# Optimization experiments

Hardware: AMD Instinct MI355X
Metric: run time of the kernel (lower is better)

The kernel has to match this reference:

```python
import jax, jax.numpy as jnp
import numpy as np

T, N, D, E, O = 2, 4096, 1024, 8, 1024

def setup_inputs() -> dict:
    key = jax.random.key(0)
    k1, k2, k3 = jax.random.split(key, 3)
    x = jax.random.normal(k1, (T, N, D), dtype=jnp.float32)
    Wg = jax.random.normal(k2, (T, D, E), dtype=jnp.float32) * (1.0 / np.sqrt(D))
    We = jax.random.normal(k3, (E, D, O), dtype=jnp.float32) * (1.0 / np.sqrt(D))
    return {"x": x, "Wg": Wg, "We": We, "k": 2}


def reference(x, Wg, We, k):
    # Per-task gating logits: [T, N, E]
    logits = jnp.einsum('tnd,tde->tne', x, Wg)
    # Top-k mask per token (scatter 1.0 at top-k indices)
    _, topk_idx = jax.lax.top_k(logits, k)                      # [T, N, k]
    mask = jax.nn.one_hot(topk_idx, E, dtype=logits.dtype).sum(-2)  # [T, N, E]
    masked = mask * logits
    gates = masked / (masked.sum(-1, keepdims=True) + 1e-9)     # [T, N, E]
    # Dense expert outputs (each expert is Linear(D, O)): [T, N, E, O]
    eout = jnp.einsum('tnd,edo->tneo', x, We)
    # Weighted combine over selected experts
    out = jnp.einsum('tne,tneo->tno', gates, eout)              # [T, N, O]
    return out
```

## Files before the change

### kernel.cpp

```cpp
#include <hip/hip_runtime.h>
#include <hip/hip_bf16.h>
#include <stdint.h>

#define T_ 2
#define N_ 4096
#define D_ 1024
#define E_ 8
#define O_ 1024

#define BM 128
#define BN 128
#define BK 32

typedef __attribute__((ext_vector_type(8))) short short8;
typedef __attribute__((ext_vector_type(4))) float f32x4;

#define AS1 __attribute__((address_space(1)))
#define AS3 __attribute__((address_space(3)))

__device__ inline void gld16(const unsigned short* g, unsigned short* l) {
    __builtin_amdgcn_global_load_lds((const AS1 unsigned int*)g,
                                     (AS3 unsigned int*)l, 16, 0, 0);
}

__device__ inline unsigned short f2bf(float f) {
    union { float f; unsigned u; } v; v.f = f;
    unsigned r = v.u + 0x7fff + ((v.u >> 16) & 1);
    return (unsigned short)(r >> 16);
}

__global__ __launch_bounds__(256) void gate_kernel(
    const float* __restrict__ x, const float* __restrict__ Wg,
    unsigned short* __restrict__ xb,
    int* __restrict__ route, float2* __restrict__ gpair)
{
    __shared__ __align__(16) float WgT[E_][D_];

    int tid = threadIdx.x;
    int wave = tid >> 6, lane = tid & 63;
    int token0 = blockIdx.x * 8;
    int t = token0 >> 12;
    const float* wgb = Wg + (size_t)t * D_ * E_;

#pragma unroll
    for (int r = 0; r < 8; ++r) {
        int f = r * 1024 + tid * 4;
        float4 v = *(const float4*)(wgb + f);
        WgT[f & 7][f >> 3]             = v.x;
        WgT[(f + 1) & 7][(f + 1) >> 3] = v.y;
        WgT[(f + 2) & 7][(f + 2) >> 3] = v.z;
        WgT[(f + 3) & 7][(f + 3) >> 3] = v.w;
    }
    __syncthreads();

#pragma unroll
    for (int tl = 0; tl < 2; ++tl) {
        int token = token0 + wave * 2 + tl;
        const float* xrow = x + (size_t)token * D_;

        float4 xv[4];
#pragma unroll
        for (int c = 0; c < 4; ++c)
            xv[c] = *(const float4*)(xrow + c * 256 + lane * 4);

        float acc[E_] = {0.f, 0.f, 0.f, 0.f, 0.f, 0.f, 0.f, 0.f};
#pragma unroll
        for (int c = 0; c < 4; ++c) {
            int d0 = c * 256 + lane * 4;
            unsigned lo = f2bf(xv[c].x) | ((unsigned)f2bf(xv[c].y) << 16);
            unsigned hi = f2bf(xv[c].z) | ((unsigned)f2bf(xv[c].w) << 16);
            *(uint2*)(&xb[(size_t)token * D_ + d0]) = make_uint2(lo, hi);
#pragma unroll
            for (int e = 0; e < E_; ++e) {
                float4 w = *(const float4*)(&WgT[e][d0]);
                acc[e] += xv[c].x * w.x + xv[c].y * w.y + xv[c].z * w.z + xv[c].w * w.w;
            }
        }
#pragma unroll
        for (int off = 1; off < 64; off <<= 1) {
#pragma unroll
            for (int e = 0; e < E_; ++e) acc[e] += __shfl_xor(acc[e], off, 64);
        }

        if (lane == 0) {
            float best = acc[0]; int bi = 0;
#pragma unroll
            for (int e = 1; e < E_; ++e) if (acc[e] > best) { best = acc[e]; bi = e; }
            float sec = -INFINITY; int si = 0;
#pragma unroll
            for (int e = 0; e < E_; ++e) if (e != bi && acc[e] > sec) { sec = acc[e]; si = e; }
            float s = best + sec + 1e-9f;
            route[token] = bi | (si << 8);
            gpair[token] = make_float2(best / s, sec / s);
        }
    }
}

__global__ __launch_bounds__(256) void build_lists(
    const int* __restrict__ route, const float2* __restrict__ gpair,
    int* __restrict__ toklist, float* __restrict__ gatelist,
    int* __restrict__ counts)
{
    int g = blockIdx.x;
    int t = g >> 3, e = g & 7;
    int tid = threadIdx.x;
    int wave = tid >> 6, lane = tid & 63;

    __shared__ int waveSum[4];
    __shared__ int base;
    if (tid == 0) base = 0;

    for (int c = 0; c < N_; c += 256) {
        int n = c + tid;
        int r = route[t * N_ + n];
        int e0 = r & 255, e1 = (r >> 8) & 255;
        bool sel = (e0 == e) || (e1 == e);
        unsigned long long b = __ballot(sel);
        int pre  = __popcll(b & ((1ull << lane) - 1ull));
        if (lane == 0) waveSum[wave] = __popcll(b);
        __syncthreads();
        int woff = 0;
#pragma unroll
        for (int w = 0; w < 4; ++w) woff += (w < wave) ? waveSum[w] : 0;
        int total = waveSum[0] + waveSum[1] + waveSum[2] + waveSum[3];
        if (sel) {
            int p = base + woff + pre;
            int slot = (e0 == e) ? 0 : 1;
            toklist[g * N_ + p] = n | (slot << 16);
            float2 gp = gpair[t * N_ + n];
            gatelist[g * N_ + p] = (e0 == e) ? gp.x : gp.y;
        }
        __syncthreads();
        if (tid == 0) base += total;
    }
    __syncthreads();
    if (tid == 0) counts[g] = base;
}

__global__ __launch_bounds__(256) void pack_kernel(
    const float* __restrict__ We, unsigned short* __restrict__ Wbp)
{
    __shared__ __align__(16) unsigned short P[64 * 136];

    int b = blockIdx.x;
    int e  = b >> 7;
    int oy = (b & 127) >> 3;
    int dz = b & 7;
    int o0 = oy * 64, d0 = dz * 128;
    int tid = threadIdx.x;

#pragma unroll
    for (int r = 0; r < 32; ++r) {
        int lin = r * 256 + tid;
        int dd = lin >> 6, oo = lin & 63;
        P[oo * 136 + dd] = f2bf(We[((size_t)(e * D_ + d0 + dd)) * O_ + o0 + oo]);
    }
    __syncthreads();

#pragma unroll
    for (int w = 0; w < 4; ++w) {
        int ci = w * 256 + tid;
        int oo = ci >> 4, dc = ci & 15;
        uint4 v = *(const uint4*)&P[oo * 136 + dc * 8];
        int o = o0 + oo;
        int ot = o >> 7, nn = o & 127;
        unsigned short* dst =
            Wbp + ((size_t)((e * 8 + ot) * 128 + nn)) * D_ + d0 + dc * 8;
        *(uint4*)dst = v;
    }
}

__global__ __launch_bounds__(256) void moe_gemm(
    const unsigned short* __restrict__ xb,
    const unsigned short* __restrict__ Wbp,
    const int* __restrict__ toklist, const float* __restrict__ gatelist,
    const int* __restrict__ counts, float* __restrict__ out)
{
    int lin = blockIdx.x;
    int mt  = lin >> 7;
    int u   = lin & 127;
    int xcd = u & 7;
    int v   = u >> 3;
    int g   = 2 * xcd + (v >> 3);
    int ot  = v & 7;
    int t   = g >> 3;

    int cnt = counts[g];
    int m0 = mt * BM;
    if (m0 >= cnt) return;

    __shared__ __align__(16) unsigned short As[BM * BK];
    __shared__ __align__(16) unsigned short Bs[BN * BK];
    __shared__ int   tokS[BM];
    __shared__ float gateS[BM];

    int tid = threadIdx.x;
    if (tid < BM) {
        int r = m0 + tid;
        tokS[tid]  = (r < cnt) ? toklist[g * N_ + r]  : -1;
        gateS[tid] = (r < cnt) ? gatelist[g * N_ + r] : 0.f;
    }
    __syncthreads();

    int wave = tid >> 6, lane = tid & 63;
    int lr = lane >> 2;
    int sg = (lane & 3) ^ (lr & 3);
    int c0 = wave * 2, c1 = c0 + 1;
    int ar0 = c0 * 16 + lr, ar1 = c1 * 16 + lr;
    int tok0 = max(tokS[ar0], 0) & 0xFFFF;
    int tok1 = max(tokS[ar1], 0) & 0xFFFF;
    const unsigned short* ag0 = xb + ((size_t)(t * N_ + tok0)) * D_ + sg * 8;
    const unsigned short* ag1 = xb + ((size_t)(t * N_ + tok1)) * D_ + sg * 8;
    const unsigned short* wb  = Wbp + ((size_t)((g & 7) * 8 + ot) * 128) * D_;
    const unsigned short* bg0 = wb + (size_t)ar0 * D_ + sg * 8;
    const unsigned short* bg1 = wb + (size_t)ar1 * D_ + sg * 8;
    unsigned short* la0 = &As[c0 * 512];
    unsigned short* la1 = &As[c1 * 512];
    unsigned short* lb0 = &Bs[c0 * 512];
    unsigned short* lb1 = &Bs[c1 * 512];

    int fr = lane & 15, q = lane >> 4;
    int wm = (wave & 1) * 64, wn = (wave >> 1) * 64;
    int fp = (q ^ (fr & 3)) * 8;

    f32x4 acc[4][4];
#pragma unroll
    for (int mi = 0; mi < 4; ++mi)
#pragma unroll
        for (int ni = 0; ni < 4; ++ni) acc[mi][ni] = (f32x4){0.f, 0.f, 0.f, 0.f};

    for (int k0 = 0; k0 < D_; k0 += BK) {
        gld16(ag0 + k0, la0);
        gld16(ag1 + k0, la1);
        gld16(bg0 + k0, lb0);
        gld16(bg1 + k0, lb1);
        __syncthreads();

        short8 af[4], bf[4];
#pragma unroll
        for (int mi = 0; mi < 4; ++mi)
            af[mi] = *(const short8*)(&As[(wm + mi * 16 + fr) * BK + fp]);
#pragma unroll
        for (int ni = 0; ni < 4; ++ni)
            bf[ni] = *(const short8*)(&Bs[(wn + ni * 16 + fr) * BK + fp]);
#pragma unroll
        for (int mi = 0; mi < 4; ++mi)
#pragma unroll
            for (int ni = 0; ni < 4; ++ni)
                acc[mi][ni] = __builtin_amdgcn_mfma_f32_16x16x32_bf16(
                    af[mi], bf[ni], acc[mi][ni], 0, 0, 0);
        __syncthreads();
    }

    float* outb = out + (size_t)t * N_ * O_;
    int ncol = ot * 128 + wn + fr;
#pragma unroll
    for (int mi = 0; mi < 4; ++mi) {
#pragma unroll
        for (int r = 0; r < 4; ++r) {
            int ml = wm + mi * 16 + q * 4 + r;
            int ent = tokS[ml];
            if (ent >= 0) {
                int tok  = ent & 0xFFFF;
                int slot = ent >> 16;
                float gate = gateS[ml];
#pragma unroll
                for (int ni = 0; ni < 4; ++ni) {
                    unsigned short* p =
                        (unsigned short*)(outb + (size_t)tok * O_ + ncol + ni * 16);
                    p[slot] = f2bf(gate * acc[mi][ni][r]);
                }
            }
        }
    }
}

__global__ __launch_bounds__(256) void combine_kernel(float* __restrict__ out)
{
    size_t i = ((size_t)blockIdx.x * 256 + threadIdx.x) * 4;
    unsigned* po = (unsigned*)out;
    uint4 v = *(uint4*)(po + i);
    float4 r;
    union { unsigned u; float f; } a, b;
#define CMB(comp, src) a.u = (src) << 16; b.u = (src) & 0xFFFF0000u; comp = a.f + b.f
    CMB(r.x, v.x); CMB(r.y, v.y); CMB(r.z, v.z); CMB(r.w, v.w);
#undef CMB
    *(float4*)(out + i) = r;
}

extern "C" void kernel_launch(void* const* d_in, const int* in_sizes, int n_in,
                              void* d_out, int out_size, void* d_ws, size_t ws_size,
                              hipStream_t stream)
{
    const float* x  = (const float*)d_in[0];
    const float* Wg = (const float*)d_in[1];
    const float* We = (const float*)d_in[2];
    float* out = (float*)d_out;

    char* ws = (char*)d_ws;
    unsigned short* xb   = (unsigned short*)(ws);
    unsigned short* Wbp  = (unsigned short*)(ws + 16777216);
    int*   toklist       = (int*)  (ws + 33554432);
    float* gatelist      = (float*)(ws + 33816576);
    int*   counts        = (int*)  (ws + 34078720);
    int*   route         = (int*)  (ws + 34078976);
    float2* gpair        = (float2*)(ws + 34111744);

    gate_kernel<<<(T_ * N_) / 8, 256, 0, stream>>>(x, Wg, xb, route, gpair);
    build_lists<<<T_ * E_, 256, 0, stream>>>(route, gpair, toklist, gatelist, counts);
    pack_kernel<<<E_ * (O_ / 64) * (D_ / 128), 256, 0, stream>>>(We, Wbp);
    moe_gemm<<<(N_ / BM) * 8 * (T_ * E_), 256, 0, stream>>>(
        xb, Wbp, toklist, gatelist, counts, out);
    combine_kernel<<<((size_t)T_ * N_ * O_) / (256 * 4), 256, 0, stream>>>(out);
}
```

Measured before the change: 194.7 us.

## Double-buffer LDS tiles in expert GEMM and adjust LDS swizzle

The A and B LDS tiles become ping-pong buffers. The next k-slice's global-to-LDS loads are issued after the current fragments are read into registers, so loads overlap with the MFMA work, and one barrier per iteration is removed. The XOR swizzle for LDS writes and fragment reads changes from row&3 to (row>>1)&3 to reduce bank conflicts on short8 reads. This doubles tile LDS use, which may lower occupancy, and it relies on the barrier waiting for the async LDS loads to finish.

```diff
diff --git a/kernel.cpp b/kernel.cpp
--- a/kernel.cpp
+++ b/kernel.cpp
@@ -189,8 +189,8 @@
     int m0 = mt * BM;
     if (m0 >= cnt) return;
 
-    __shared__ __align__(16) unsigned short As[BM * BK];
-    __shared__ __align__(16) unsigned short Bs[BN * BK];
+    __shared__ __align__(16) unsigned short As[2][BM * BK];
+    __shared__ __align__(16) unsigned short Bs[2][BN * BK];
     __shared__ int   tokS[BM];
     __shared__ float gateS[BM];
 
@@ -204,7 +204,7 @@
 
     int wave = tid >> 6, lane = tid & 63;
     int lr = lane >> 2;
-    int sg = (lane & 3) ^ (lr & 3);
+    int sg = (lane & 3) ^ ((lane >> 3) & 3);
     int c0 = wave * 2, c1 = c0 + 1;
     int ar0 = c0 * 16 + lr, ar1 = c1 * 16 + lr;
     int tok0 = max(tokS[ar0], 0) & 0xFFFF;
@@ -214,14 +214,10 @@
     const unsigned short* wb  = Wbp + ((size_t)((g & 7) * 8 + ot) * 128) * D_;
     const unsigned short* bg0 = wb + (size_t)ar0 * D_ + sg * 8;
     const unsigned short* bg1 = wb + (size_t)ar1 * D_ + sg * 8;
-    unsigned short* la0 = &As[c0 * 512];
-    unsigned short* la1 = &As[c1 * 512];
-    unsigned short* lb0 = &Bs[c0 * 512];
-    unsigned short* lb1 = &Bs[c1 * 512];
 
     int fr = lane & 15, q = lane >> 4;
     int wm = (wave & 1) * 64, wn = (wave >> 1) * 64;
-    int fp = (q ^ (fr & 3)) * 8;
+    int fp = (q ^ ((fr >> 1) & 3)) * 8;
 
     f32x4 acc[4][4];
 #pragma unroll
@@ -229,27 +225,37 @@
 #pragma unroll
         for (int ni = 0; ni < 4; ++ni) acc[mi][ni] = (f32x4){0.f, 0.f, 0.f, 0.f};
 
-    for (int k0 = 0; k0 < D_; k0 += BK) {
-        gld16(ag0 + k0, la0);
-        gld16(ag1 + k0, la1);
-        gld16(bg0 + k0, lb0);
-        gld16(bg1 + k0, lb1);
+    gld16(ag0, &As[0][c0 * 512]);
+    gld16(ag1, &As[0][c1 * 512]);
+    gld16(bg0, &Bs[0][c0 * 512]);
+    gld16(bg1, &Bs[0][c1 * 512]);
+
+    for (int k = 0; k < D_ / BK; ++k) {
+        int p = k & 1;
         __syncthreads();
 
         short8 af[4], bf[4];
 #pragma unroll
         for (int mi = 0; mi < 4; ++mi)
-            af[mi] = *(const short8*)(&As[(wm + mi * 16 + fr) * BK + fp]);
+            af[mi] = *(const short8*)(&As[p][(wm + mi * 16 + fr) * BK + fp]);
 #pragma unroll
         for (int ni = 0; ni < 4; ++ni)
-            bf[ni] = *(const short8*)(&Bs[(wn + ni * 16 + fr) * BK + fp]);
+            bf[ni] = *(const short8*)(&Bs[p][(wn + ni * 16 + fr) * BK + fp]);
+
+        if (k + 1 < D_ / BK) {
+            int ko = (k + 1) * BK;
+            gld16(ag0 + ko, &As[p ^ 1][c0 * 512]);
+            gld16(ag1 + ko, &As[p ^ 1][c1 * 512]);
+            gld16(bg0 + ko, &Bs[p ^ 1][c0 * 512]);
+            gld16(bg1 + ko, &Bs[p ^ 1][c1 * 512]);
+        }
+
 #pragma unroll
         for (int mi = 0; mi < 4; ++mi)
 #pragma unroll
             for (int ni = 0; ni < 4; ++ni)
                 acc[mi][ni] = __builtin_amdgcn_mfma_f32_16x16x32_bf16(
                     af[mi], bf[ni], acc[mi][ni], 0, 0, 0);
-        __syncthreads();
     }
 
     float* outb = out + (size_t)t * N_ * O_;
@@ -266,9 +272,9 @@
                 float gate = gateS[ml];
 #pragma unroll
                 for (int ni = 0; ni < 4; ++ni) {
-                    unsigned short* p =
+                    unsigned short* p2 =
                         (unsigned short*)(outb + (size_t)tok * O_ + ncol + ni * 16);
-                    p[slot] = f2bf(gate * acc[mi][ni][r]);
+                    p2[slot] = f2bf(gate * acc[mi][ni][r]);
                 }
             }
         }
```

Result: no change. 198.1 us (+1.7%).

## Widen GEMM N tile to 256 and switch to 32x32x16 MFMA

Applied to the files above, without the earlier changes.

The grouped MoE GEMM tile grows from 128x128 to 128x256, so each block loads an A tile once for twice as many output columns. The MFMA shape changes from 16x16x32 to 32x32x16, and the LDS swizzle and epilogue row mapping are reworked to match. The packed weight layout becomes plain row-major per expert, and the launch bounds now request two blocks per CU. The larger tile raises register and LDS use per block and halves the number of blocks, which may reduce occupancy and parallelism when per-expert token counts are small.

```diff
diff --git a/kernel.cpp b/kernel.cpp
--- a/kernel.cpp
+++ b/kernel.cpp
@@ -9,11 +9,11 @@
 #define O_ 1024
 
 #define BM 128
-#define BN 128
+#define BN2 256
 #define BK 32
 
 typedef __attribute__((ext_vector_type(8))) short short8;
-typedef __attribute__((ext_vector_type(4))) float f32x4;
+typedef __attribute__((ext_vector_type(16))) float f32x16;
 
 #define AS1 __attribute__((address_space(1)))
 #define AS3 __attribute__((address_space(3)))
@@ -163,26 +163,24 @@
         int oo = ci >> 4, dc = ci & 15;
         uint4 v = *(const uint4*)&P[oo * 136 + dc * 8];
         int o = o0 + oo;
-        int ot = o >> 7, nn = o & 127;
-        unsigned short* dst =
-            Wbp + ((size_t)((e * 8 + ot) * 128 + nn)) * D_ + d0 + dc * 8;
+        unsigned short* dst = Wbp + ((size_t)(e * O_ + o)) * D_ + d0 + dc * 8;
         *(uint4*)dst = v;
     }
 }
 
-__global__ __launch_bounds__(256) void moe_gemm(
+__global__ __launch_bounds__(256, 2) void moe_gemm(
     const unsigned short* __restrict__ xb,
     const unsigned short* __restrict__ Wbp,
     const int* __restrict__ toklist, const float* __restrict__ gatelist,
     const int* __restrict__ counts, float* __restrict__ out)
 {
     int lin = blockIdx.x;
-    int mt  = lin >> 7;
-    int u   = lin & 127;
+    int mt  = lin >> 6;
+    int u   = lin & 63;
     int xcd = u & 7;
     int v   = u >> 3;
-    int g   = 2 * xcd + (v >> 3);
-    int ot  = v & 7;
+    int g   = 2 * xcd + (v >> 2);
+    int ot  = v & 3;
     int t   = g >> 3;
 
     int cnt = counts[g];
@@ -190,7 +188,7 @@
     if (m0 >= cnt) return;
 
     __shared__ __align__(16) unsigned short As[BM * BK];
-    __shared__ __align__(16) unsigned short Bs[BN * BK];
+    __shared__ __align__(16) unsigned short Bs[BN2 * BK];
     __shared__ int   tokS[BM];
     __shared__ float gateS[BM];
 
@@ -204,71 +202,78 @@
 
     int wave = tid >> 6, lane = tid & 63;
     int lr = lane >> 2;
-    int sg = (lane & 3) ^ (lr & 3);
-    int c0 = wave * 2, c1 = c0 + 1;
-    int ar0 = c0 * 16 + lr, ar1 = c1 * 16 + lr;
-    int tok0 = max(tokS[ar0], 0) & 0xFFFF;
-    int tok1 = max(tokS[ar1], 0) & 0xFFFF;
-    const unsigned short* ag0 = xb + ((size_t)(t * N_ + tok0)) * D_ + sg * 8;
-    const unsigned short* ag1 = xb + ((size_t)(t * N_ + tok1)) * D_ + sg * 8;
-    const unsigned short* wb  = Wbp + ((size_t)((g & 7) * 8 + ot) * 128) * D_;
-    const unsigned short* bg0 = wb + (size_t)ar0 * D_ + sg * 8;
-    const unsigned short* bg1 = wb + (size_t)ar1 * D_ + sg * 8;
-    unsigned short* la0 = &As[c0 * 512];
-    unsigned short* la1 = &As[c1 * 512];
-    unsigned short* lb0 = &Bs[c0 * 512];
-    unsigned short* lb1 = &Bs[c1 * 512];
-
-    int fr = lane & 15, q = lane >> 4;
-    int wm = (wave & 1) * 64, wn = (wave >> 1) * 64;
-    int fp = (q ^ (fr & 3)) * 8;
-
-    f32x4 acc[4][4];
-#pragma unroll
-    for (int mi = 0; mi < 4; ++mi)
-#pragma unroll
-        for (int ni = 0; ni < 4; ++ni) acc[mi][ni] = (f32x4){0.f, 0.f, 0.f, 0.f};
+    int sg = (lane & 3) ^ ((lane >> 3) & 3);
+    int a0 = wave * 32 + lr, a1 = a0 + 16;
+    int tokA0 = max(tokS[a0], 0) & 0xFFFF;
+    int tokA1 = max(tokS[a1], 0) & 0xFFFF;
+    const unsigned short* ag0 = xb + ((size_t)(t * N_ + tokA0)) * D_ + sg * 8;
+    const unsigned short* ag1 = xb + ((size_t)(t * N_ + tokA1)) * D_ + sg * 8;
+    const unsigned short* wb  = Wbp + ((size_t)((g & 7) * O_ + ot * BN2)) * D_;
+    const unsigned short* bg[4];
+#pragma unroll
+    for (int i = 0; i < 4; ++i)
+        bg[i] = wb + (size_t)(wave * 64 + i * 16 + lr) * D_ + sg * 8;
+
+    int fm = lane & 31, kg = lane >> 5;
+    int wm = (wave & 1) * 64, wn = (wave >> 1) * 128;
+    int sA = (fm >> 1) & 3;
+
+    f32x16 acc[2][4];
+#pragma unroll
+    for (int mi = 0; mi < 2; ++mi)
+#pragma unroll
+        for (int ni = 0; ni < 4; ++ni)
+#pragma unroll
+            for (int r = 0; r < 16; ++r) acc[mi][ni][r] = 0.f;
 
     for (int k0 = 0; k0 < D_; k0 += BK) {
-        gld16(ag0 + k0, la0);
-        gld16(ag1 + k0, la1);
-        gld16(bg0 + k0, lb0);
-        gld16(bg1 + k0, lb1);
+        gld16(ag0 + k0, &As[(wave * 2) * 512]);
+        gld16(ag1 + k0, &As[(wave * 2 + 1) * 512]);
+#pragma unroll
+        for (int i = 0; i < 4; ++i)
+            gld16(bg[i] + k0, &Bs[(wave * 4 + i) * 512]);
         __syncthreads();
 
-        short8 af[4], bf[4];
-#pragma unroll
-        for (int mi = 0; mi < 4; ++mi)
-            af[mi] = *(const short8*)(&As[(wm + mi * 16 + fr) * BK + fp]);
-#pragma unroll
-        for (int ni = 0; ni < 4; ++ni)
-            bf[ni] = *(const short8*)(&Bs[(wn + ni * 16 + fr) * BK + fp]);
-#pragma unroll
-        for (int mi = 0; mi < 4; ++mi)
+        short8 af[2][2], bf[4][2];
+#pragma unroll
+        for (int kk = 0; kk < 2; ++kk) {
+            int pos = ((kk * 2 + kg) ^ sA) * 8;
+#pragma unroll
+            for (int mi = 0; mi < 2; ++mi)
+                af[mi][kk] = *(const short8*)(&As[(wm + mi * 32 + fm) * BK + pos]);
 #pragma unroll
             for (int ni = 0; ni < 4; ++ni)
-                acc[mi][ni] = __builtin_amdgcn_mfma_f32_16x16x32_bf16(
-                    af[mi], bf[ni], acc[mi][ni], 0, 0, 0);
+                bf[ni][kk] = *(const short8*)(&Bs[(wn + ni * 32 + fm) * BK + pos]);
+        }
         __syncthreads();
+
+#pragma unroll
+        for (int kk = 0; kk < 2; ++kk)
+#pragma unroll
+            for (int mi = 0; mi < 2; ++mi)
+#pragma unroll
+                for (int ni = 0; ni < 4; ++ni)
+                    acc[mi][ni] = __builtin_amdgcn_mfma_f32_32x32x16_bf16(
+                        af[mi][kk], bf[ni][kk], acc[mi][ni], 0, 0, 0);
     }
 
     float* outb = out + (size_t)t * N_ * O_;
-    int ncol = ot * 128 + wn + fr;
-#pragma unroll
-    for (int mi = 0; mi < 4; ++mi) {
-#pragma unroll
-        for (int r = 0; r < 4; ++r) {
-            int ml = wm + mi * 16 + q * 4 + r;
-            int ent = tokS[ml];
+    int ncol0 = ot * BN2 + wn + fm;
+#pragma unroll
+    for (int mi = 0; mi < 2; ++mi) {
+#pragma unroll
+        for (int reg = 0; reg < 16; ++reg) {
+            int rl = wm + mi * 32 + (reg & 3) + 8 * (reg >> 2) + 4 * kg;
+            int ent = tokS[rl];
             if (ent >= 0) {
                 int tok  = ent & 0xFFFF;
                 int slot = ent >> 16;
-                float gate = gateS[ml];
+                float gate = gateS[rl];
 #pragma unroll
                 for (int ni = 0; ni < 4; ++ni) {
                     unsigned short* p =
-                        (unsigned short*)(outb + (size_t)tok * O_ + ncol + ni * 16);
-                    p[slot] = f2bf(gate * acc[mi][ni][r]);
+                        (unsigned short*)(outb + (size_t)tok * O_ + ncol0 + ni * 32);
+                    p[slot] = f2bf(gate * acc[mi][ni][reg]);
                 }
             }
         }
@@ -309,7 +314,7 @@
     gate_kernel<<<(T_ * N_) / 8, 256, 0, stream>>>(x, Wg, xb, route, gpair);
     build_lists<<<T_ * E_, 256, 0, stream>>>(route, gpair, toklist, gatelist, counts);
     pack_kernel<<<E_ * (O_ / 64) * (D_ / 128), 256, 0, stream>>>(We, Wbp);
-    moe_gemm<<<(N_ / BM) * 8 * (T_ * E_), 256, 0, stream>>>(
+    moe_gemm<<<(N_ / BM) * (O_ / BN2) * (T_ * E_), 256, 0, stream>>>(
         xb, Wbp, toklist, gatelist, counts, out);
     combine_kernel<<<((size_t)T_ * N_ * O_) / (256 * 4), 256, 0, stream>>>(out);
 }
```

Result: slower. 210.9 us (+8.3%).
